# Kernel optimization log

Hardware: AMD Instinct MI355X
Metric: run time of the kernel (lower is better)

## Reference

```python
import jax, jax.numpy as jnp
import numpy as np

N_NODES = 50000
N_EDGES = 800000
D_IN = 128
D_SH = 16
D_OUT = 128
N_PATHS = 64


def setup_inputs() -> dict:
    key = jax.random.key(0)
    k1, k2, k3, k4, k5, k6, k7, k8 = jax.random.split(key, 8)
    x = jax.random.normal(k1, (N_NODES, D_IN), dtype=jnp.float32)
    sh = jax.random.normal(k2, (N_EDGES, D_SH), dtype=jnp.float32)
    coeff = jax.random.normal(k3, (N_PATHS,), dtype=jnp.float32)
    src = jax.random.randint(k4, (N_EDGES,), 0, N_NODES, dtype=jnp.int64)
    dst = jax.random.randint(k5, (N_EDGES,), 0, N_NODES, dtype=jnp.int64)
    ki = jax.random.randint(k6, (N_PATHS,), 0, D_IN, dtype=jnp.int32)
    kj = jax.random.randint(k7, (N_PATHS,), 0, D_SH, dtype=jnp.int32)
    ko = jax.random.randint(k8, (N_PATHS,), 0, D_OUT, dtype=jnp.int32)
    return {"x": x, "sh": sh, "coeff": coeff, "src": src, "dst": dst,
            "ki": ki, "kj": kj, "ko": ko}


def reference(x, sh, coeff, src, dst, ki, kj, ko):
    # 1) gather: index_select node features by edge source -> [E, D_in]
    xg = x[src]
    # 2) segmented tensor product: sum over sparse paths p of
    #    coeff[p] * xg[:, ki[p]] * sh[:, kj[p]] accumulated into output slot ko[p]
    vals = coeff[None, :] * xg[:, ki] * sh[:, kj]          # [E, P]
    msg = jnp.zeros((sh.shape[0], D_OUT), dtype=x.dtype).at[:, ko].add(vals)  # [E, D_out]
    # 3) scatter_add messages into per-node output -> [N, D_out]
    out = jnp.zeros((x.shape[0], D_OUT), dtype=x.dtype).at[dst].add(msg)
    return out
```

## Files before the change

kernel.cpp:

```cpp
#include <hip/hip_runtime.h>
#include <hip/hip_fp16.h>

#define N_NODES 50000
#define N_EDGES 800000
#define D_IN    128
#define D_SH    16
#define D_OUT   128
#define N_PATHS 64

#define SEGN    128
#define NSEG    391
#define NSEGP   512
#define CAPE    2560
#define EPB     3125
#define BINB    256
#define XCB     3125
#define BLK     256
#define BLK2    512

#define OFF_META 2048
#define OFF_SH16 (OFF_META + NSEG*CAPE*4)
#define OFF_XCH  (OFF_SH16 + NSEG*CAPE*32)

__global__ __launch_bounds__(BLK) void bin_kernel(
        const float* __restrict__ x, const int* __restrict__ ki,
        const float* __restrict__ sh, const int* __restrict__ src,
        const int* __restrict__ dst, int* __restrict__ segcnt,
        int* __restrict__ meta, __half* __restrict__ sh16,
        __half* __restrict__ xc_h) {
    __shared__ int lcnt[NSEGP];
    __shared__ int lstart[NSEGP];
    __shared__ int lofs[NSEGP];
    __shared__ int gbase[NSEGP];
    __shared__ unsigned short sorted_[EPB];
    const int tid = threadIdx.x;

    if (blockIdx.x < BINB) {
        const int e0 = blockIdx.x * EPB;
        for (int s = tid; s < NSEGP; s += BLK) lcnt[s] = 0;
        __syncthreads();
        for (int i = tid; i < EPB; i += BLK)
            atomicAdd(&lcnt[dst[e0 + i] >> 7], 1);
        __syncthreads();
        if (tid < 64) {
            int b8 = tid * 8, v[8], s0 = 0;
            #pragma unroll
            for (int k = 0; k < 8; ++k) { v[k] = lcnt[b8 + k]; s0 += v[k]; }
            int run = s0;
            #pragma unroll
            for (int off = 1; off < 64; off <<= 1) {
                int y = __shfl_up(run, off);
                if (tid >= off) run += y;
            }
            int acc = run - s0;
            #pragma unroll
            for (int k = 0; k < 8; ++k) {
                lstart[b8 + k] = acc; lofs[b8 + k] = acc; acc += v[k];
            }
        } else {
            for (int s = tid - 64; s < NSEG; s += BLK - 64) {
                int c = lcnt[s];
                gbase[s] = c ? atomicAdd(&segcnt[s], c) : 0;
            }
        }
        __syncthreads();
        for (int i = tid; i < EPB; i += BLK) {
            int r = atomicAdd(&lofs[dst[e0 + i] >> 7], 1);
            sorted_[r] = (unsigned short)i;
        }
        __syncthreads();
        for (int j = tid; j < EPB; j += BLK) {
            int i = sorted_[j];
            int e = e0 + i;
            int d = dst[e];
            int s = d >> 7;
            int pos = gbase[s] + (j - lstart[s]);
            if (pos < CAPE) {
                size_t gi = (size_t)s * CAPE + pos;
                meta[gi] = src[e] | ((d & 127) << 16);
                const float4* shv = (const float4*)(sh + (size_t)e * D_SH);
                float4 f0 = shv[0], f1 = shv[1], f2 = shv[2], f3 = shv[3];
                union { __half2 h[8]; int4 v[2]; } u;
                u.h[0] = __floats2half2_rn(f0.x, f0.y);
                u.h[1] = __floats2half2_rn(f0.z, f0.w);
                u.h[2] = __floats2half2_rn(f1.x, f1.y);
                u.h[3] = __floats2half2_rn(f1.z, f1.w);
                u.h[4] = __floats2half2_rn(f2.x, f2.y);
                u.h[5] = __floats2half2_rn(f2.z, f2.w);
                u.h[6] = __floats2half2_rn(f3.x, f3.y);
                u.h[7] = __floats2half2_rn(f3.z, f3.w);
                int4* dp = (int4*)(sh16 + gi * 16);
                dp[0] = u.v[0]; dp[1] = u.v[1];
            }
        }
    } else {
        const int b2   = blockIdx.x - BINB;
        const int lane = tid & 63;
        const int w    = tid >> 6;
        const int nb   = b2 * 16 + w * 4;
        const int kil  = ki[lane];
        float x0 = x[(size_t)(nb + 0) * D_IN + kil];
        float x1 = x[(size_t)(nb + 1) * D_IN + kil];
        float x2 = x[(size_t)(nb + 2) * D_IN + kil];
        float x3 = x[(size_t)(nb + 3) * D_IN + kil];
        xc_h[(size_t)(nb + 0) * N_PATHS + lane] = __float2half_rn(x0);
        xc_h[(size_t)(nb + 1) * N_PATHS + lane] = __float2half_rn(x1);
        xc_h[(size_t)(nb + 2) * N_PATHS + lane] = __float2half_rn(x2);
        xc_h[(size_t)(nb + 3) * N_PATHS + lane] = __float2half_rn(x3);
    }
}

__global__ __launch_bounds__(BLK2) void node_kernel(
        const int* __restrict__ segcnt, const int* __restrict__ meta,
        const __half* __restrict__ sh16, const __half* __restrict__ xc_h,
        const float* __restrict__ coeff, const int* __restrict__ kj,
        const int* __restrict__ ko, float* __restrict__ out) {
    __shared__ int cnt_l[SEGN];
    __shared__ int nstart[SEGN];
    __shared__ int ncur[SEGN];
    __shared__ unsigned short csr[CAPE];
    __shared__ int metash[CAPE];
    __shared__ float srow[BLK2 / 64][D_OUT];
    const int tid  = threadIdx.x;
    const int lane = tid & 63;
    const int w    = tid >> 6;
    const int seg  = blockIdx.x;
    const int n_e  = min(segcnt[seg], CAPE);
    const size_t mb = (size_t)seg * CAPE;
    const __half* shb = sh16 + mb * 16;

    for (int s = tid; s < SEGN; s += BLK2) cnt_l[s] = 0;
    __syncthreads();
    for (int i = tid; i < n_e; i += BLK2) {
        int m = meta[mb + i];
        metash[i] = m;
        atomicAdd(&cnt_l[(m >> 16) & 127], 1);
    }
    __syncthreads();
    if (tid < 64) {
        int b2 = tid * 2;
        int v0 = cnt_l[b2], v1 = cnt_l[b2 + 1];
        int s0 = v0 + v1;
        int run = s0;
        #pragma unroll
        for (int off = 1; off < 64; off <<= 1) {
            int y = __shfl_up(run, off);
            if (tid >= off) run += y;
        }
        int acc = run - s0;
        nstart[b2] = acc;          ncur[b2] = acc;
        nstart[b2 + 1] = acc + v0; ncur[b2 + 1] = acc + v0;
    }
    __syncthreads();
    for (int i = tid; i < n_e; i += BLK2) {
        int dl = (metash[i] >> 16) & 127;
        int r = atomicAdd(&ncur[dl], 1);
        csr[r] = (unsigned short)i;
    }
    __syncthreads();

    const int   kj_p = kj[lane];
    const int   ko_p = ko[lane];
    const float c_p  = coeff[lane];

    for (int nl = w; nl < SEGN; nl += BLK2 / 64) {
        const int node = seg * SEGN + nl;
        if (node >= N_NODES) break;
        const int st = nstart[nl];
        const int en = (nl + 1 < SEGN) ? nstart[nl + 1] : n_e;
        float acc = 0.0f;
        int j = st;
        for (; j + 4 <= en; j += 4) {
            int i0 = csr[j], i1 = csr[j + 1], i2 = csr[j + 2], i3 = csr[j + 3];
            int m0 = metash[i0], m1 = metash[i1];
            int m2 = metash[i2], m3 = metash[i3];
            float x0 = __half2float(xc_h[(size_t)(m0 & 0xFFFF) * N_PATHS + lane]);
            float s0 = __half2float(shb[(size_t)i0 * 16 + kj_p]);
            float x1 = __half2float(xc_h[(size_t)(m1 & 0xFFFF) * N_PATHS + lane]);
            float s1 = __half2float(shb[(size_t)i1 * 16 + kj_p]);
            float x2 = __half2float(xc_h[(size_t)(m2 & 0xFFFF) * N_PATHS + lane]);
            float s2 = __half2float(shb[(size_t)i2 * 16 + kj_p]);
            float x3 = __half2float(xc_h[(size_t)(m3 & 0xFFFF) * N_PATHS + lane]);
            float s3 = __half2float(shb[(size_t)i3 * 16 + kj_p]);
            acc += x0 * s0; acc += x1 * s1; acc += x2 * s2; acc += x3 * s3;
        }
        for (; j < en; ++j) {
            int i0 = csr[j];
            int m0 = metash[i0];
            acc += __half2float(xc_h[(size_t)(m0 & 0xFFFF) * N_PATHS + lane])
                 * __half2float(shb[(size_t)i0 * 16 + kj_p]);
        }
        acc *= c_p;
        srow[w][lane]      = 0.0f;
        srow[w][lane + 64] = 0.0f;
        atomicAdd(&srow[w][ko_p], acc);
        float r0 = srow[w][lane];
        float r1 = srow[w][lane + 64];
        float* orow = out + (size_t)node * D_OUT;
        orow[lane]      = r0;
        orow[lane + 64] = r1;
    }
}

extern "C" void kernel_launch(void* const* d_in, const int* in_sizes, int n_in,
                              void* d_out, int out_size, void* d_ws, size_t ws_size,
                              hipStream_t stream) {
    const float* x     = (const float*)d_in[0];
    const float* sh    = (const float*)d_in[1];
    const float* coeff = (const float*)d_in[2];
    const int*   src   = (const int*)d_in[3];
    const int*   dst   = (const int*)d_in[4];
    const int*   ki    = (const int*)d_in[5];
    const int*   kj    = (const int*)d_in[6];
    const int*   ko    = (const int*)d_in[7];
    float* out = (float*)d_out;

    char* p = (char*)d_ws;
    int*    segcnt = (int*)p;
    int*    meta   = (int*)(p + OFF_META);
    __half* sh16   = (__half*)(p + OFF_SH16);
    __half* xc_h   = (__half*)(p + OFF_XCH);
    (void)ws_size;

    hipMemsetAsync(segcnt, 0, 2048, stream);
    bin_kernel<<<BINB + XCB, BLK, 0, stream>>>(
        x, ki, sh, src, dst, segcnt, meta, sh16, xc_h);
    node_kernel<<<NSEG, BLK2, 0, stream>>>(
        segcnt, meta, sh16, xc_h, coeff, kj, ko, out);
}
```

Measured before the change: 225.7 us.

## Split node kernel into quarter-segment blocks with packed CSR and 8-way unroll

Each 128-node segment is now handled by four 256-thread blocks, each owning 32 nodes, so 1564 blocks are launched instead of 391 and the GPU is filled better. Each block rescans the segment's meta twice and keeps only its own edges, building a CSR that stores source ids and edge indices directly, which removes the metash indirection. The gather loop is unrolled 8-wide with a masked tail to keep more loads in flight. In exchange, every segment's meta is read four times, and QCAP caps a quarter at 1024 edges.

```diff
diff --git a/kernel.cpp b/kernel.cpp
--- a/kernel.cpp
+++ b/kernel.cpp
@@ -16,7 +16,10 @@
 #define BINB    256
 #define XCB     3125
 #define BLK     256
-#define BLK2    512
+
+#define QN      32
+#define QCAP    1024
+#define NQB     (NSEG * 4)
 
 #define OFF_META 2048
 #define OFF_SH16 (OFF_META + NSEG*CAPE*4)
@@ -110,52 +113,57 @@
     }
 }
 
-__global__ __launch_bounds__(BLK2) void node_kernel(
+__global__ __launch_bounds__(BLK) void node_kernel(
         const int* __restrict__ segcnt, const int* __restrict__ meta,
         const __half* __restrict__ sh16, const __half* __restrict__ xc_h,
         const float* __restrict__ coeff, const int* __restrict__ kj,
         const int* __restrict__ ko, float* __restrict__ out) {
-    __shared__ int cnt_l[SEGN];
-    __shared__ int nstart[SEGN];
-    __shared__ int ncur[SEGN];
-    __shared__ unsigned short csr[CAPE];
-    __shared__ int metash[CAPE];
-    __shared__ float srow[BLK2 / 64][D_OUT];
+    __shared__ int cnt_l[QN];
+    __shared__ int nstart[QN + 1];
+    __shared__ int ncur[QN];
+    __shared__ unsigned short csr_src[QCAP];
+    __shared__ unsigned short csr_idx[QCAP];
+    __shared__ float srow[BLK / 64][D_OUT];
     const int tid  = threadIdx.x;
     const int lane = tid & 63;
     const int w    = tid >> 6;
-    const int seg  = blockIdx.x;
+    const int seg  = blockIdx.x >> 2;
+    const int q    = blockIdx.x & 3;
+    const int nb_l = q * QN;
     const int n_e  = min(segcnt[seg], CAPE);
     const size_t mb = (size_t)seg * CAPE;
     const __half* shb = sh16 + mb * 16;
 
-    for (int s = tid; s < SEGN; s += BLK2) cnt_l[s] = 0;
-    __syncthreads();
-    for (int i = tid; i < n_e; i += BLK2) {
-        int m = meta[mb + i];
-        metash[i] = m;
-        atomicAdd(&cnt_l[(m >> 16) & 127], 1);
-    }
-    __syncthreads();
-    if (tid < 64) {
-        int b2 = tid * 2;
-        int v0 = cnt_l[b2], v1 = cnt_l[b2 + 1];
-        int s0 = v0 + v1;
-        int run = s0;
+    if (tid < QN) cnt_l[tid] = 0;
+    __syncthreads();
+    for (int i = tid; i < n_e; i += BLK) {
+        unsigned int u = (unsigned)(((meta[mb + i] >> 16) & 127) - nb_l);
+        if (u < QN) atomicAdd(&cnt_l[u], 1);
+    }
+    __syncthreads();
+    if (tid < QN) {
+        int v = cnt_l[tid];
+        int run = v;
         #pragma unroll
-        for (int off = 1; off < 64; off <<= 1) {
+        for (int off = 1; off < QN; off <<= 1) {
             int y = __shfl_up(run, off);
             if (tid >= off) run += y;
         }
-        int acc = run - s0;
-        nstart[b2] = acc;          ncur[b2] = acc;
-        nstart[b2 + 1] = acc + v0; ncur[b2 + 1] = acc + v0;
-    }
-    __syncthreads();
-    for (int i = tid; i < n_e; i += BLK2) {
-        int dl = (metash[i] >> 16) & 127;
-        int r = atomicAdd(&ncur[dl], 1);
-        csr[r] = (unsigned short)i;
+        nstart[tid] = run - v;
+        ncur[tid]   = run - v;
+        if (tid == QN - 1) nstart[QN] = run;
+    }
+    __syncthreads();
+    for (int i = tid; i < n_e; i += BLK) {
+        int m = meta[mb + i];
+        unsigned int u = (unsigned)(((m >> 16) & 127) - nb_l);
+        if (u < QN) {
+            int r = atomicAdd(&ncur[u], 1);
+            if (r < QCAP) {
+                csr_src[r] = (unsigned short)(m & 0xFFFF);
+                csr_idx[r] = (unsigned short)i;
+            }
+        }
     }
     __syncthreads();
 
@@ -163,42 +171,52 @@
     const int   ko_p = ko[lane];
     const float c_p  = coeff[lane];
 
-    for (int nl = w; nl < SEGN; nl += BLK2 / 64) {
-        const int node = seg * SEGN + nl;
-        if (node >= N_NODES) break;
-        const int st = nstart[nl];
-        const int en = (nl + 1 < SEGN) ? nstart[nl + 1] : n_e;
+    #pragma unroll 1
+    for (int k = 0; k < QN / (BLK / 64); ++k) {
+        const int c    = w * (QN / (BLK / 64)) + k;
+        const int node = seg * SEGN + nb_l + c;
+        const int st   = nstart[c];
+        const int en   = nstart[c + 1];
         float acc = 0.0f;
         int j = st;
-        for (; j + 4 <= en; j += 4) {
-            int i0 = csr[j], i1 = csr[j + 1], i2 = csr[j + 2], i3 = csr[j + 3];
-            int m0 = metash[i0], m1 = metash[i1];
-            int m2 = metash[i2], m3 = metash[i3];
-            float x0 = __half2float(xc_h[(size_t)(m0 & 0xFFFF) * N_PATHS + lane]);
-            float s0 = __half2float(shb[(size_t)i0 * 16 + kj_p]);
-            float x1 = __half2float(xc_h[(size_t)(m1 & 0xFFFF) * N_PATHS + lane]);
-            float s1 = __half2float(shb[(size_t)i1 * 16 + kj_p]);
-            float x2 = __half2float(xc_h[(size_t)(m2 & 0xFFFF) * N_PATHS + lane]);
-            float s2 = __half2float(shb[(size_t)i2 * 16 + kj_p]);
-            float x3 = __half2float(xc_h[(size_t)(m3 & 0xFFFF) * N_PATHS + lane]);
-            float s3 = __half2float(shb[(size_t)i3 * 16 + kj_p]);
-            acc += x0 * s0; acc += x1 * s1; acc += x2 * s2; acc += x3 * s3;
-        }
-        for (; j < en; ++j) {
-            int i0 = csr[j];
-            int m0 = metash[i0];
-            acc += __half2float(xc_h[(size_t)(m0 & 0xFFFF) * N_PATHS + lane])
-                 * __half2float(shb[(size_t)i0 * 16 + kj_p]);
+        for (; j + 8 <= en; j += 8) {
+            float xv[8], sv[8];
+            #pragma unroll
+            for (int u8 = 0; u8 < 8; ++u8) {
+                int s = csr_src[j + u8];
+                int i = csr_idx[j + u8];
+                xv[u8] = __half2float(xc_h[(size_t)s * N_PATHS + lane]);
+                sv[u8] = __half2float(shb[(size_t)i * 16 + kj_p]);
+            }
+            #pragma unroll
+            for (int u8 = 0; u8 < 8; ++u8) acc += xv[u8] * sv[u8];
+        }
+        if (j < en) {
+            float xv[8], sv[8];
+            #pragma unroll
+            for (int u8 = 0; u8 < 8; ++u8) {
+                int jj = j + u8;
+                int jc = jj < en ? jj : st;
+                int s = csr_src[jc];
+                int i = csr_idx[jc];
+                xv[u8] = __half2float(xc_h[(size_t)s * N_PATHS + lane]);
+                sv[u8] = __half2float(shb[(size_t)i * 16 + kj_p]);
+            }
+            #pragma unroll
+            for (int u8 = 0; u8 < 8; ++u8)
+                if (j + u8 < en) acc += xv[u8] * sv[u8];
         }
         acc *= c_p;
-        srow[w][lane]      = 0.0f;
-        srow[w][lane + 64] = 0.0f;
-        atomicAdd(&srow[w][ko_p], acc);
-        float r0 = srow[w][lane];
-        float r1 = srow[w][lane + 64];
-        float* orow = out + (size_t)node * D_OUT;
-        orow[lane]      = r0;
-        orow[lane + 64] = r1;
+        if (node < N_NODES) {
+            srow[w][lane]      = 0.0f;
+            srow[w][lane + 64] = 0.0f;
+            atomicAdd(&srow[w][ko_p], acc);
+            float r0 = srow[w][lane];
+            float r1 = srow[w][lane + 64];
+            float* orow = out + (size_t)node * D_OUT;
+            orow[lane]      = r0;
+            orow[lane + 64] = r1;
+        }
     }
 }
 
@@ -225,6 +243,6 @@
     hipMemsetAsync(segcnt, 0, 2048, stream);
     bin_kernel<<<BINB + XCB, BLK, 0, stream>>>(
         x, ki, sh, src, dst, segcnt, meta, sh16, xc_h);
-    node_kernel<<<NSEG, BLK2, 0, stream>>>(
+    node_kernel<<<NQB, BLK, 0, stream>>>(
         segcnt, meta, sh16, xc_h, coeff, kj, ko, out);
 }
```

Result: faster. 208.5 us (-7.6%).

## Replace per-node CSR sort with shared-memory atomic accumulation per segment

Applied to the files above, without the earlier changes.

The node kernel no longer builds a per-node CSR inside each segment. Instead it streams edges in groups of 64, broadcasts each edge's metadata with readlane, and atomically adds each path product into a 128x128 shared accumulator tile, which is then written out with float4 stores. The coefficient multiply moves into the x-precompute step of the bin kernel, so it is folded into the fp16 gathered features. This removes the counting, scan and scatter phases and their syncs, but adds heavy LDS atomic traffic with possible conflicts on shared ko slots, and a 64KB shared tile that limits occupancy.

```diff
diff --git a/kernel.cpp b/kernel.cpp
--- a/kernel.cpp
+++ b/kernel.cpp
@@ -24,6 +24,7 @@
 
 __global__ __launch_bounds__(BLK) void bin_kernel(
         const float* __restrict__ x, const int* __restrict__ ki,
+        const float* __restrict__ coeff,
         const float* __restrict__ sh, const int* __restrict__ src,
         const int* __restrict__ dst, int* __restrict__ segcnt,
         int* __restrict__ meta, __half* __restrict__ sh16,
@@ -99,28 +100,24 @@
         const int w    = tid >> 6;
         const int nb   = b2 * 16 + w * 4;
         const int kil  = ki[lane];
+        const float cl = coeff[lane];
         float x0 = x[(size_t)(nb + 0) * D_IN + kil];
         float x1 = x[(size_t)(nb + 1) * D_IN + kil];
         float x2 = x[(size_t)(nb + 2) * D_IN + kil];
         float x3 = x[(size_t)(nb + 3) * D_IN + kil];
-        xc_h[(size_t)(nb + 0) * N_PATHS + lane] = __float2half_rn(x0);
-        xc_h[(size_t)(nb + 1) * N_PATHS + lane] = __float2half_rn(x1);
-        xc_h[(size_t)(nb + 2) * N_PATHS + lane] = __float2half_rn(x2);
-        xc_h[(size_t)(nb + 3) * N_PATHS + lane] = __float2half_rn(x3);
+        xc_h[(size_t)(nb + 0) * N_PATHS + lane] = __float2half_rn(cl * x0);
+        xc_h[(size_t)(nb + 1) * N_PATHS + lane] = __float2half_rn(cl * x1);
+        xc_h[(size_t)(nb + 2) * N_PATHS + lane] = __float2half_rn(cl * x2);
+        xc_h[(size_t)(nb + 3) * N_PATHS + lane] = __float2half_rn(cl * x3);
     }
 }
 
 __global__ __launch_bounds__(BLK2) void node_kernel(
         const int* __restrict__ segcnt, const int* __restrict__ meta,
         const __half* __restrict__ sh16, const __half* __restrict__ xc_h,
-        const float* __restrict__ coeff, const int* __restrict__ kj,
-        const int* __restrict__ ko, float* __restrict__ out) {
-    __shared__ int cnt_l[SEGN];
-    __shared__ int nstart[SEGN];
-    __shared__ int ncur[SEGN];
-    __shared__ unsigned short csr[CAPE];
-    __shared__ int metash[CAPE];
-    __shared__ float srow[BLK2 / 64][D_OUT];
+        const int* __restrict__ kj, const int* __restrict__ ko,
+        float* __restrict__ out) {
+    __shared__ float acc[SEGN][D_OUT];
     const int tid  = threadIdx.x;
     const int lane = tid & 63;
     const int w    = tid >> 6;
@@ -129,76 +126,66 @@
     const size_t mb = (size_t)seg * CAPE;
     const __half* shb = sh16 + mb * 16;
 
-    for (int s = tid; s < SEGN; s += BLK2) cnt_l[s] = 0;
+    const int kj_p = kj[lane];
+    const int ko_p = ko[lane];
+
+    float4* accv = (float4*)&acc[0][0];
+    #pragma unroll
+    for (int i = 0; i < (SEGN * D_OUT / 4) / BLK2; ++i)
+        accv[tid + i * BLK2] = make_float4(0.f, 0.f, 0.f, 0.f);
     __syncthreads();
-    for (int i = tid; i < n_e; i += BLK2) {
-        int m = meta[mb + i];
-        metash[i] = m;
-        atomicAdd(&cnt_l[(m >> 16) & 127], 1);
+
+    const int ngrp = n_e >> 6;
+    for (int g = w; g < ngrp; g += BLK2 / 64) {
+        const int jb = g << 6;
+        const int mreg = meta[mb + jb + lane];
+        #pragma unroll
+        for (int s8 = 0; s8 < 8; ++s8) {
+            float xv[8], sv[8];
+            int   dl[8];
+            #pragma unroll
+            for (int u = 0; u < 8; ++u) {
+                int m = __builtin_amdgcn_readlane(mreg, s8 * 8 + u);
+                int s = m & 0xFFFF;
+                dl[u] = (m >> 16) & 127;
+                xv[u] = __half2float(xc_h[(size_t)s * N_PATHS + lane]);
+                sv[u] = __half2float(shb[(size_t)(jb + s8 * 8 + u) * 16 + kj_p]);
+            }
+            #pragma unroll
+            for (int u = 0; u < 8; ++u)
+                atomicAdd(&acc[dl[u]][ko_p], xv[u] * sv[u]);
+        }
+    }
+    const int jt  = ngrp << 6;
+    const int rem = n_e - jt;
+    if (rem > 0) {
+        const int mreg = (jt + lane < n_e) ? meta[mb + jt + lane] : 0;
+        float xv[8], sv[8];
+        int   dl[8];
+        #pragma unroll
+        for (int t = 0; t < 8; ++t) {
+            int u  = w + t * 8;
+            bool go = u < rem;
+            int m  = __shfl(mreg, go ? u : 0);
+            int s  = m & 0xFFFF;
+            dl[t]  = (m >> 16) & 127;
+            xv[t] = go ? __half2float(xc_h[(size_t)s * N_PATHS + lane]) : 0.f;
+            sv[t] = go ? __half2float(shb[(size_t)(jt + u) * 16 + kj_p]) : 0.f;
+        }
+        #pragma unroll
+        for (int t = 0; t < 8; ++t)
+            if (w + t * 8 < rem)
+                atomicAdd(&acc[dl[t]][ko_p], xv[t] * sv[t]);
     }
     __syncthreads();
-    if (tid < 64) {
-        int b2 = tid * 2;
-        int v0 = cnt_l[b2], v1 = cnt_l[b2 + 1];
-        int s0 = v0 + v1;
-        int run = s0;
-        #pragma unroll
-        for (int off = 1; off < 64; off <<= 1) {
-            int y = __shfl_up(run, off);
-            if (tid >= off) run += y;
-        }
-        int acc = run - s0;
-        nstart[b2] = acc;          ncur[b2] = acc;
-        nstart[b2 + 1] = acc + v0; ncur[b2 + 1] = acc + v0;
-    }
-    __syncthreads();
-    for (int i = tid; i < n_e; i += BLK2) {
-        int dl = (metash[i] >> 16) & 127;
-        int r = atomicAdd(&ncur[dl], 1);
-        csr[r] = (unsigned short)i;
-    }
-    __syncthreads();
-
-    const int   kj_p = kj[lane];
-    const int   ko_p = ko[lane];
-    const float c_p  = coeff[lane];
-
-    for (int nl = w; nl < SEGN; nl += BLK2 / 64) {
-        const int node = seg * SEGN + nl;
-        if (node >= N_NODES) break;
-        const int st = nstart[nl];
-        const int en = (nl + 1 < SEGN) ? nstart[nl + 1] : n_e;
-        float acc = 0.0f;
-        int j = st;
-        for (; j + 4 <= en; j += 4) {
-            int i0 = csr[j], i1 = csr[j + 1], i2 = csr[j + 2], i3 = csr[j + 3];
-            int m0 = metash[i0], m1 = metash[i1];
-            int m2 = metash[i2], m3 = metash[i3];
-            float x0 = __half2float(xc_h[(size_t)(m0 & 0xFFFF) * N_PATHS + lane]);
-            float s0 = __half2float(shb[(size_t)i0 * 16 + kj_p]);
-            float x1 = __half2float(xc_h[(size_t)(m1 & 0xFFFF) * N_PATHS + lane]);
-            float s1 = __half2float(shb[(size_t)i1 * 16 + kj_p]);
-            float x2 = __half2float(xc_h[(size_t)(m2 & 0xFFFF) * N_PATHS + lane]);
-            float s2 = __half2float(shb[(size_t)i2 * 16 + kj_p]);
-            float x3 = __half2float(xc_h[(size_t)(m3 & 0xFFFF) * N_PATHS + lane]);
-            float s3 = __half2float(shb[(size_t)i3 * 16 + kj_p]);
-            acc += x0 * s0; acc += x1 * s1; acc += x2 * s2; acc += x3 * s3;
-        }
-        for (; j < en; ++j) {
-            int i0 = csr[j];
-            int m0 = metash[i0];
-            acc += __half2float(xc_h[(size_t)(m0 & 0xFFFF) * N_PATHS + lane])
-                 * __half2float(shb[(size_t)i0 * 16 + kj_p]);
-        }
-        acc *= c_p;
-        srow[w][lane]      = 0.0f;
-        srow[w][lane + 64] = 0.0f;
-        atomicAdd(&srow[w][ko_p], acc);
-        float r0 = srow[w][lane];
-        float r1 = srow[w][lane + 64];
-        float* orow = out + (size_t)node * D_OUT;
-        orow[lane]      = r0;
-        orow[lane + 64] = r1;
+
+    float4* out4 = (float4*)(out + (size_t)seg * SEGN * D_OUT);
+    const int rowbase = seg * SEGN;
+    #pragma unroll
+    for (int i = 0; i < (SEGN * D_OUT / 4) / BLK2; ++i) {
+        int idx  = tid + i * BLK2;
+        int node = rowbase + (idx >> 5);
+        if (node < N_NODES) out4[idx] = accv[idx];
     }
 }
 
@@ -222,9 +209,9 @@
     __half* xc_h   = (__half*)(p + OFF_XCH);
     (void)ws_size;
 
-    hipMemsetAsync(segcnt, 0, 2048, stream);
+    hipMemsetAsync(p, 0, 2048, stream);
     bin_kernel<<<BINB + XCB, BLK, 0, stream>>>(
-        x, ki, sh, src, dst, segcnt, meta, sh16, xc_h);
+        x, ki, coeff, sh, src, dst, segcnt, meta, sh16, xc_h);
     node_kernel<<<NSEG, BLK2, 0, stream>>>(
-        segcnt, meta, sh16, xc_h, coeff, kj, ko, out);
+        segcnt, meta, sh16, xc_h, kj, ko, out);
 }
```

Result: slower. 506.1 us (+124.3%).
